# Performance work log

Hardware: AMD Instinct MI355X
Metric: run time of the kernel (lower is better)

Reference implementation:

```python
import jax, jax.numpy as jnp
import numpy as np

M = 8      # bits // 8 experts
SUB = 8    # sub-code width per expert
HID = 256  # expert output classes (2**SUB)
BITS = 64
NCLS = 100
NUM_FLIP = (BITS // 32) ** 2  # 4


def _bit_flip(x, template, key):
    # torch: rand.argsort(-1) -> shuffledTemplate = template[idx]; x[mask] *= -1
    rand = jax.random.uniform(key, x.shape)
    idx = jnp.argsort(rand, axis=-1)
    mask = template[idx]
    return jnp.where(mask, -x, x)


def _map_net(x, W1, b1, W2, b2):
    # m independent Linear(8,256)->SiLU->Linear(256,256) experts over contiguous chunks
    N = x.shape[0]
    xs = x.reshape(N, M, SUB)
    h = jax.nn.silu(jnp.einsum('nmi,mih->nmh', xs, W1) + b1)
    return jnp.einsum('nmh,mho->nmo', h, W2) + b2  # [N, M, HID]


def setup_inputs() -> dict:
    key = jax.random.key(0)
    ks = jax.random.split(key, 10)
    N = 32768
    x = jax.random.normal(ks[0], (N, BITS), jnp.float32)
    # multi-label targets, guarantee >=1 positive per row (meanWeight divides by row sum)
    y = (jax.random.uniform(ks[1], (N, NCLS)) < 0.1).astype(jnp.int32)
    lab = jax.random.randint(ks[2], (N,), 0, NCLS)
    y = y.at[jnp.arange(N), lab].set(1)
    centroids = (jax.random.uniform(ks[3], (NCLS, BITS)) > 0.5).astype(jnp.float32)
    permIdx = jax.random.permutation(ks[4], BITS)

    def make_template(k):
        t = jnp.zeros(BITS, bool).at[:NUM_FLIP].set(True)
        return jax.random.permutation(k, t)

    template_map = make_template(ks[5])
    template_raw = make_template(ks[6])
    W1 = jax.random.normal(ks[7], (M, SUB, HID), jnp.float32) / np.sqrt(SUB)
    b1 = jnp.zeros((M, HID), jnp.float32)
    W2 = jax.random.normal(ks[8], (M, HID, HID), jnp.float32) / np.sqrt(HID)
    b2 = jnp.zeros((M, HID), jnp.float32)
    return dict(x=x, y=y, centroids=centroids, permIdx=permIdx,
                template_map=template_map, template_raw=template_raw,
                W1=W1, b1=b1, W2=W2, b2=b2)


def reference(x, y, centroids, permIdx, template_map, template_raw, W1, b1, W2, b2):
    N = x.shape[0]
    multiplier = 2 ** jnp.arange(SUB)  # [8]
    kmap, kraw = jax.random.split(jax.random.key(1))

    xp = x[:, permIdx]  # permuted codes [N, BITS]
    x_det = jax.lax.stop_gradient(xp)

    # ---- mapLoss path (x detached; mapper params still trained; dropout in eval) ----
    logits_map = _map_net(_bit_flip(x_det, template_map, kmap), W1, b1, W2, b2)  # [N,M,HID]
    raw_flipped = _bit_flip(x_det, template_raw, kraw)
    binary = raw_flipped.reshape(N, M, SUB) > 0
    target = (binary * multiplier).sum(-1)  # [N, M] decimal sub-codes
    lse = jax.nn.logsumexp(logits_map, axis=-1)
    picked = jnp.take_along_axis(logits_map, target[..., None], axis=-1)[..., 0]
    mapLoss = (lse - picked).mean(0).sum()  # sum over m of per-chunk CE means
    hitRate = (logits_map.argmax(-1) == target).astype(jnp.float32).mean()

    # ---- netLoss path (mapper on non-detached x, no flip; centers detached) ----
    hashCenter = jax.lax.stop_gradient(centroids[:, permIdx])  # [C, BITS]
    centerBits = hashCenter > 0
    centerTarget = (centerBits.reshape(NCLS, M, SUB) * multiplier).sum(-1)  # [C, M]
    logits_net = _map_net(xp, W1, b1, W2, b2)  # [N, M, HID]
    lse2 = jax.nn.logsumexp(logits_net, axis=-1)  # [N, M]
    # picked2[n,m,c] = logits_net[n, m, centerTarget[c, m]]
    picked2 = logits_net[:, jnp.arange(M)[:, None], centerTarget.T]  # [N, M, C]
    ce = lse2[..., None] - picked2  # [N, M, C]
    mask = y > 0
    w = mask.astype(jnp.float32)
    w = w / w.sum(-1, keepdims=True)  # meanWeight (mask * meanWeight == meanWeight)
    netLoss = (ce * w[:, None, :]).sum() / N

    # ---- codes-to-center Hamming distance, masked mean over (n, c) with y>0 ----
    xb = (xp > 0).astype(jnp.float32)
    cb = centerBits.astype(jnp.float32)
    ham = xb.sum(-1, keepdims=True) + cb.sum(-1)[None, :] - 2.0 * (xb @ cb.T)  # [N, C]
    mf = mask.astype(jnp.float32)
    codesToCenterDistance = (ham * mf).sum() / mf.sum()

    total = netLoss + mapLoss
    return (total, netLoss, mapLoss, hitRate, codesToCenterDistance)
```

## Files before the change

### kernel.cpp

```cpp
#include <hip/hip_runtime.h>
#include <stdint.h>

#define NR 32768
#define MM 8
#define NCLS 100
#define HALFN 1048576u
#define HSS 260
#define LGS 260
#define PSS 12

#define LOG2E 1.4426950408889634f
#define LN2F  0.6931471805599453f

typedef _Float16 h8 __attribute__((ext_vector_type(8)));
typedef _Float16 h4 __attribute__((ext_vector_type(4)));
typedef float f4 __attribute__((ext_vector_type(4)));
typedef unsigned long long ull;

__host__ __device__ inline void tf2x32(uint32_t k0, uint32_t k1, uint32_t x0, uint32_t x1,
                                       uint32_t& o0, uint32_t& o1) {
  uint32_t ks0 = k0, ks1 = k1, ks2 = k0 ^ k1 ^ 0x1BD11BDAu;
  x0 += ks0; x1 += ks1;
#define TFR(r) { x0 += x1; x1 = (x1 << r) | (x1 >> (32 - r)); x1 ^= x0; }
  TFR(13) TFR(15) TFR(26) TFR(6)  x0 += ks1; x1 += ks2 + 1u;
  TFR(17) TFR(29) TFR(16) TFR(24) x0 += ks2; x1 += ks0 + 2u;
  TFR(13) TFR(15) TFR(26) TFR(6)  x0 += ks0; x1 += ks1 + 3u;
  TFR(17) TFR(29) TFR(16) TFR(24) x0 += ks1; x1 += ks2 + 4u;
  TFR(13) TFR(15) TFR(26) TFR(6)  x0 += ks2; x1 += ks0 + 5u;
#undef TFR
  o0 = x0; o1 = x1;
}

__device__ inline int load_tmpl(const void* p, int lane) {
  const unsigned* pi = (const unsigned*)p;
  unsigned w = pi[lane];
  ull okF = __ballot(w == 0u || w == 0x3F800000u);
  ull onF = __ballot(w == 0x3F800000u);
  ull okI = __ballot(w <= 1u);
  ull onI = __ballot(w == 1u);
  if (okF == ~0ull && __popcll(onF) == 4) return (w == 0x3F800000u) ? 1 : 0;
  if (okI == ~0ull && __popcll(onI) == 4) return (int)w;
  const unsigned char* pb = (const unsigned char*)p;
  return pb[lane] ? 1 : 0;
}

__device__ inline uint32_t packh2(float a, float b) {
  union { _Float16 h[2]; uint32_t u; } cv;
  cv.h[0] = (_Float16)a; cv.h[1] = (_Float16)b;
  return cv.u;
}

__device__ inline ull flip_mask(ull tmask, uint32_t key) {
  ull fm = 0;
  while (tmask) {
    int p = __ffsll((long long)tmask) - 1;
    tmask &= tmask - 1;
    uint32_t kp = (uint32_t)__builtin_amdgcn_readlane((int)key, p);
    fm |= 1ull << __popcll(__ballot(key < kp));
  }
  return fm;
}

__global__ __launch_bounds__(256) void stage1p(
    const float* __restrict__ x, const int* __restrict__ y, const int* __restrict__ perm,
    const void* tmap, const void* traw,
    uint32_t km0, uint32_t km1, uint32_t kr0, uint32_t kr1,
    const float* __restrict__ W2, const float* __restrict__ W1,
    const float* __restrict__ B1, const float* __restrict__ B2,
    const float* __restrict__ centroids,
    _Float16* __restrict__ Wp, _Float16* __restrict__ Wp1, float* __restrict__ B2s,
    ull* __restrict__ cb64,
    uint32_t* __restrict__ xp16, uint32_t* __restrict__ xm16,
    ull* __restrict__ targ, ull* __restrict__ xb,
    float* __restrict__ winv, unsigned char* __restrict__ poslist, int* __restrict__ nposA) {
  int b = blockIdx.x, tid = threadIdx.x;
  if (b >= 2048) {
    int pb = b - 2048;
    if (pb < 256) {
      int gid = pb * 256 + tid;
      int lane6 = gid & 63, frag = gid >> 6;
      int NT = frag & 15, kt = (frag >> 4) & 7, m = frag >> 7;
      int q = lane6 >> 4, lr = lane6 & 15;
      const float* src = W2 + (size_t)m * 65536 + (size_t)(kt * 32 + q * 8) * 256 + NT * 16 + lr;
      h8 v;
#pragma unroll
      for (int j = 0; j < 8; j++) v[j] = (_Float16)src[j * 256];
      *(h8*)(Wp + (size_t)gid * 8) = v;
    } else if (pb < 288) {
      int idx = (pb - 256) * 256 + tid;
      int lane = idx & 63, t = (idx >> 6) & 15, m = idx >> 10;
      int q = lane >> 4, lr = lane & 15;
      h8 v;
#pragma unroll
      for (int j = 0; j < 8; j++) {
        float val = 0.0f;
        if (q == 0) val = W1[(size_t)(m * 8 + j) * 256 + t * 16 + lr] * LOG2E;
        else if (q == 1 && j == 0) val = B1[m * 256 + t * 16 + lr] * LOG2E;
        v[j] = (_Float16)val;
      }
      *(h8*)(Wp1 + (size_t)idx * 8) = v;
    } else if (pb < 313) {
      int c = (pb - 288) * 4 + (tid >> 6);
      int lane = tid & 63;
      ull bits = __ballot(centroids[c * 64 + perm[lane]] > 0.0f);
      if (lane == 0 && c < NCLS) cb64[c] = bits;
    } else {
#pragma unroll
      for (int j = 0; j < 8; j++) B2s[tid * 8 + j] = B2[tid * 8 + j] * LOG2E;
    }
    return;
  }

  int wv = tid >> 6, lane = tid & 63;
  int tm = load_tmpl(tmap, lane);
  int tr = load_tmpl(traw, lane);
  ull tmm = __ballot(tm != 0);
  ull trm = __ballot(tr != 0);
  int pv = perm[lane];

  int nbase = b * 8 + wv * 2;
  uint32_t bmv[4], brv[4];
  {
    uint32_t iA = (uint32_t)(nbase * 64 + lane);
    uint32_t iB = iA + 64u;
    tf2x32(km0, km1, iA, iA + HALFN, bmv[0], bmv[2]);
    tf2x32(kr0, kr1, iA, iA + HALFN, brv[0], brv[2]);
    tf2x32(km0, km1, iB, iB + HALFN, bmv[1], bmv[3]);
    tf2x32(kr0, kr1, iB, iB + HALFN, brv[1], brv[3]);
  }
  const int nn[4] = {nbase, nbase + 1, nbase + 16384, nbase + 16385};
#pragma unroll
  for (int rr = 0; rr < 4; rr++) {
    int n = nn[rr];
    float xpv = x[(size_t)n * 64 + pv];
    uint32_t kmk = ((bmv[rr] >> 9) << 6) | (uint32_t)lane;
    uint32_t krk = ((brv[rr] >> 9) << 6) | (uint32_t)lane;
    ull fm = flip_mask(tmm, kmk);
    ull fr = flip_mask(trm, krk);
    float xmv = ((fm >> lane) & 1ull) ? -xpv : xpv;
    float rfv = ((fr >> lane) & 1ull) ? -xpv : xpv;
    float xp_o = __shfl_xor(xpv, 1);
    float xm_o = __shfl_xor(xmv, 1);
    if ((lane & 1) == 0) {
      xp16[n * 32 + (lane >> 1)] = packh2(xpv, xp_o);
      xm16[n * 32 + (lane >> 1)] = packh2(xmv, xm_o);
    }
    ull t64 = __ballot(rfv > 0.0f);
    ull b64v = __ballot(xpv > 0.0f);

    int c1 = y[(size_t)n * NCLS + lane] > 0;
    int c2 = (lane < NCLS - 64) ? (y[(size_t)n * NCLS + 64 + lane] > 0) : 0;
    ull p0 = __ballot(c1);
    ull p1 = __ballot(c2);
    int cnt0 = __popcll(p0);
    float cnt = (float)(cnt0 + __popcll(p1));

    unsigned char* pl = poslist + (size_t)n * 64;
    ull below = (lane == 0) ? 0ull : (~0ull >> (64 - lane));
    if (c1) pl[__popcll(p0 & below)] = (unsigned char)lane;
    if (c2) pl[cnt0 + __popcll(p1 & below)] = (unsigned char)(64 + lane);

    if (lane == 0) {
      targ[n] = t64;
      xb[n] = b64v;
      winv[n] = 1.0f / cnt;
      nposA[n] = cnt0 + __popcll(p1);
    }
  }
}

__global__ __launch_bounds__(512, 8) void mapnet8(
    const uint32_t* __restrict__ Xm16, const uint32_t* __restrict__ Xp16,
    const _Float16* __restrict__ Wp1, const _Float16* __restrict__ Wp,
    const float* __restrict__ B2s,
    const ull* __restrict__ targ, const float* __restrict__ winv,
    const unsigned char* __restrict__ poslist, const int* __restrict__ nposA,
    const ull* __restrict__ cb64, const ull* __restrict__ xb,
    float* __restrict__ accbuf) {
  __shared__ union {
    _Float16 h[64 * HSS];
    float lg[32 * LGS];
  } u;
  __shared__ float ps[64 * PSS];
  __shared__ float pm[64 * PSS];
  __shared__ float mvA[64];
  __shared__ int   tA[64];
  __shared__ float sl[3];
  const int tid = threadIdx.x, lane = tid & 63, wv = tid >> 6;
  const int q = lane >> 4, lr = lane & 15;
  const int m = blockIdx.y, pass = blockIdx.z;
  const int n0 = blockIdx.x * 64;
  if (tid < 3) sl[tid] = 0.0f;

  if (pass == 2) {
    __syncthreads();
    int flat = blockIdx.y * 512 + blockIdx.x;
    int n = flat * 8 + wv;
    ull xv = xb[n];
    float px = (float)__popcll(xv);
    int np = nposA[n];
    float hs = 0.0f;
    if (lane < np) {
      int c = poslist[(size_t)n * 64 + lane];
      ull cb = cb64[c];
      hs = px + (float)__popcll(cb) - 2.0f * (float)__popcll(xv & cb);
    }
#pragma unroll
    for (int off = 1; off < 64; off <<= 1) hs += __shfl_xor(hs, off);
    if (lane == 0) {
      atomicAdd(&sl[0], hs);
      atomicAdd(&sl[1], (float)np);
    }
    __syncthreads();
    if (tid == 0) {
      float* slot = accbuf + (flat & 127) * 8;
      atomicAdd(&slot[3], sl[0]);
      atomicAdd(&slot[4], sl[1]);
    }
    return;
  }

  const uint32_t* Xin = pass ? Xp16 : Xm16;

  const int rb = wv & 3, tbase = (wv >> 2) * 8;
  h8 af;
  {
    const _Float16* xsrc = (const _Float16*)(Xin + (size_t)(n0 + rb * 16 + lr) * 32) + m * 8;
    h8 xv = *(const h8*)xsrc;
    h8 zero = {(_Float16)0.0f, (_Float16)0.0f, (_Float16)0.0f, (_Float16)0.0f,
               (_Float16)0.0f, (_Float16)0.0f, (_Float16)0.0f, (_Float16)0.0f};
    af = (q == 0) ? xv : zero;
    if (q == 1) af[0] = (_Float16)1.0f;
  }
#pragma unroll 4
  for (int tt = 0; tt < 8; tt++) {
    int t = tbase + tt;
    h8 wfrag = *(const h8*)(Wp1 + ((size_t)(m * 16 + t) * 64 + lane) * 8);
    f4 z = __builtin_amdgcn_mfma_f32_16x16x32_f16(wfrag, af, (f4){0.f, 0.f, 0.f, 0.f}, 0, 0, 0);
    h4 pk;
#pragma unroll
    for (int reg = 0; reg < 4; reg++) {
      float z2 = z[reg];
      pk[reg] = (_Float16)(z2 * __builtin_amdgcn_rcpf(1.0f + __builtin_amdgcn_exp2f(-z2)));
    }
    *(h4*)(u.h + (size_t)(rb * 16 + lr) * HSS + t * 16 + q * 4) = pk;
  }
  __syncthreads();

  f4 acc4[4][2];
  {
    f4 bv0 = *(const f4*)(B2s + m * 256 + wv * 32 + q * 4);
    f4 bv1 = *(const f4*)(B2s + m * 256 + wv * 32 + 16 + q * 4);
#pragma unroll
    for (int rt = 0; rt < 4; rt++) { acc4[rt][0] = bv0; acc4[rt][1] = bv1; }
  }
  const size_t wbase = (size_t)m * 65536;
#pragma unroll 2
  for (int kt = 0; kt < 8; kt++) {
    h8 bh0 = *(const h8*)(Wp + wbase + (((size_t)kt * 16 + wv * 2 + 0) * 64 + lane) * 8);
    h8 bh1 = *(const h8*)(Wp + wbase + (((size_t)kt * 16 + wv * 2 + 1) * 64 + lane) * 8);
#pragma unroll
    for (int rt = 0; rt < 4; rt++) {
      const _Float16* p = u.h + (size_t)(rt * 16 + lr) * HSS + kt * 32 + q * 8;
      h4 lo = *(const h4*)p;
      h4 hi = *(const h4*)(p + 4);
      h8 ah = __builtin_shufflevector(lo, hi, 0, 1, 2, 3, 4, 5, 6, 7);
      acc4[rt][0] = __builtin_amdgcn_mfma_f32_16x16x32_f16(bh0, ah, acc4[rt][0], 0, 0, 0);
      acc4[rt][1] = __builtin_amdgcn_mfma_f32_16x16x32_f16(bh1, ah, acc4[rt][1], 0, 0, 0);
    }
  }

  float rsum[4], rmax[4];
#pragma unroll
  for (int rt = 0; rt < 4; rt++) {
    f4 l0 = acc4[rt][0], l1 = acc4[rt][1];
    float s = 0.0f;
#pragma unroll
    for (int reg = 0; reg < 4; reg++)
      s += __builtin_amdgcn_exp2f(l0[reg]) + __builtin_amdgcn_exp2f(l1[reg]);
    rsum[rt] = s;
    if (pass == 0) {
      float mv = fmaxf(l0[0], l1[0]);
#pragma unroll
      for (int reg = 1; reg < 4; reg++) mv = fmaxf(mv, fmaxf(l0[reg], l1[reg]));
      rmax[rt] = mv;
    }
  }
#pragma unroll
  for (int rt = 0; rt < 4; rt++) {
    rsum[rt] += __shfl_xor(rsum[rt], 16);
    rsum[rt] += __shfl_xor(rsum[rt], 32);
  }
  if (pass == 0) {
#pragma unroll
    for (int rt = 0; rt < 4; rt++) {
      rmax[rt] = fmaxf(rmax[rt], __shfl_xor(rmax[rt], 16));
      rmax[rt] = fmaxf(rmax[rt], __shfl_xor(rmax[rt], 32));
    }
  }
  if (lane < 16) {
#pragma unroll
    for (int rt = 0; rt < 4; rt++) {
      ps[(rt * 16 + lane) * PSS + wv] = rsum[rt];
      if (pass == 0) pm[(rt * 16 + lane) * PSS + wv] = rmax[rt];
    }
  }

  if (pass == 0) {
    __syncthreads();
    float myLse = 0.0f;
    if (tid < 64) {
      int row = tid, n = n0 + row;
      f4 s0 = *(const f4*)(ps + row * PSS);
      f4 s1 = *(const f4*)(ps + row * PSS + 4);
      f4 ss = s0 + s1;
      float s = (ss[0] + ss[1]) + (ss[2] + ss[3]);
      f4 m0 = *(const f4*)(pm + row * PSS);
      f4 m1 = *(const f4*)(pm + row * PSS + 4);
      float mv = fmaxf(fmaxf(fmaxf(m0[0], m0[1]), fmaxf(m0[2], m0[3])),
                       fmaxf(fmaxf(m1[0], m1[1]), fmaxf(m1[2], m1[3])));
      mvA[row] = mv;
      tA[row] = (int)((targ[n] >> (m * 8)) & 0xFFull);
      myLse = __builtin_amdgcn_logf(s);
    }
    __syncthreads();
    float pick = 0.0f, hit = 0.0f;
    const int cbase = wv * 32 + q * 4;
#pragma unroll
    for (int rt = 0; rt < 4; rt++) {
      int row = rt * 16 + lr;
      int d0 = tA[row] - cbase;
#pragma unroll
      for (int nt = 0; nt < 2; nt++) {
        int d = d0 - nt * 16;
        if ((unsigned)d < 4u) {
          f4 f = acc4[rt][nt];
          float v = f[0];
          v = (d == 1) ? f[1] : v;
          v = (d == 2) ? f[2] : v;
          v = (d == 3) ? f[3] : v;
          pick += v;
          hit += (v == mvA[row]) ? 1.0f : 0.0f;
        }
      }
    }
    float lossC = myLse - pick;
#pragma unroll
    for (int off = 1; off < 64; off <<= 1) {
      lossC += __shfl_xor(lossC, off);
      hit += __shfl_xor(hit, off);
    }
    if (lane == 0) {
      atomicAdd(&sl[0], lossC);
      atomicAdd(&sl[2], hit);
    }
  } else {
    float partLoss = 0.0f;
    for (int ph = 0; ph < 2; ph++) {
      __syncthreads();
#pragma unroll
      for (int rt2 = 0; rt2 < 2; rt2++) {
#pragma unroll
        for (int nt = 0; nt < 2; nt++)
#pragma unroll
          for (int reg = 0; reg < 4; reg++)
            u.lg[(rt2 * 16 + lr) * LGS + wv * 32 + nt * 16 + q * 4 + reg] =
                acc4[ph * 2 + rt2][nt][reg];
      }
      __syncthreads();
      int rl = tid >> 4;
      int grow = ph * 32 + rl;
      int n = n0 + grow;
      int cl = tid & 15;
      const float* lrow = u.lg + rl * LGS;
      int np = nposA[n];
      const unsigned char* pl = poslist + (size_t)n * 64;
      float sp = 0.0f;
      for (int j2 = cl; j2 < np; j2 += 16) {
        int c = pl[j2];
        int t = (int)((cb64[c] >> (m * 8)) & 0xFFull);
        sp += lrow[t];
      }
#pragma unroll
      for (int off = 1; off < 16; off <<= 1) sp += __shfl_xor(sp, off);
      if (cl == 0) {
        f4 s0 = *(const f4*)(ps + grow * PSS);
        f4 s1 = *(const f4*)(ps + grow * PSS + 4);
        f4 ss = s0 + s1;
        float s = (ss[0] + ss[1]) + (ss[2] + ss[3]);
        partLoss += __builtin_amdgcn_logf(s) - winv[n] * sp;
      }
    }
    partLoss += __shfl_xor(partLoss, 16);
    partLoss += __shfl_xor(partLoss, 32);
    if (lane == 0) atomicAdd(&sl[1], partLoss);
  }

  __syncthreads();
  if (tid == 0) {
    float* slot = accbuf + (blockIdx.x & 127) * 8;
    if (pass == 0) {
      atomicAdd(&slot[0], sl[0]);
      atomicAdd(&slot[2], sl[2]);
    } else {
      atomicAdd(&slot[1], sl[1]);
    }
  }
}

__global__ __launch_bounds__(128) void finalk(const float* __restrict__ accbuf, float* __restrict__ out) {
  int t = threadIdx.x;
  float v0 = accbuf[t * 8 + 0], v1 = accbuf[t * 8 + 1], v2 = accbuf[t * 8 + 2];
  float v3 = accbuf[t * 8 + 3], v4 = accbuf[t * 8 + 4];
#pragma unroll
  for (int off = 1; off < 64; off <<= 1) {
    v0 += __shfl_xor(v0, off); v1 += __shfl_xor(v1, off); v2 += __shfl_xor(v2, off);
    v3 += __shfl_xor(v3, off); v4 += __shfl_xor(v4, off);
  }
  __shared__ float s[2][5];
  if ((t & 63) == 0) {
    s[t >> 6][0] = v0; s[t >> 6][1] = v1; s[t >> 6][2] = v2; s[t >> 6][3] = v3; s[t >> 6][4] = v4;
  }
  __syncthreads();
  if (t == 0) {
    float a0 = s[0][0] + s[1][0], a1 = s[0][1] + s[1][1], a2 = s[0][2] + s[1][2];
    float a3 = s[0][3] + s[1][3], a4 = s[0][4] + s[1][4];
    float netLoss = a1 * LN2F / (float)NR;
    float mapLoss = a0 * LN2F / (float)NR;
    out[0] = netLoss + mapLoss;
    out[1] = netLoss;
    out[2] = mapLoss;
    out[3] = a2 / (float)(NR * MM);
    out[4] = a3 / a4;
  }
}

extern "C" void kernel_launch(void* const* d_in, const int* in_sizes, int n_in,
                              void* d_out, int out_size, void* d_ws, size_t ws_size,
                              hipStream_t stream) {
  const float* x = (const float*)d_in[0];
  const int* y = (const int*)d_in[1];
  const float* centroids = (const float*)d_in[2];
  const int* perm = (const int*)d_in[3];
  const void* tmap = d_in[4];
  const void* traw = d_in[5];
  const float* W1 = (const float*)d_in[6];
  const float* B1 = (const float*)d_in[7];
  const float* W2 = (const float*)d_in[8];
  const float* B2 = (const float*)d_in[9];
  float* out = (float*)d_out;

  char* w = (char*)d_ws;
  float* accbuf = (float*)w;
  uint32_t* xp16 = (uint32_t*)(w + 4096);
  uint32_t* xm16 = xp16 + (size_t)NR * 32;
  ull* targ = (ull*)(xm16 + (size_t)NR * 32);
  ull* cb64 = targ + NR;
  ull* xb = cb64 + 128;
  float* winv = (float*)(xb + NR);
  int* nposA = (int*)(winv + NR);
  unsigned char* poslist = (unsigned char*)(nposA + NR);
  _Float16* Wp = (_Float16*)(poslist + (size_t)NR * 64);
  _Float16* Wp1 = Wp + (1 << 19);
  float* B2s = (float*)(Wp1 + (1 << 16));

  hipMemsetAsync(accbuf, 0, 4096, stream);

  uint32_t a0, b0, a1, b1;
  tf2x32(0u, 1u, 0u, 2u, a0, b0);
  tf2x32(0u, 1u, 1u, 3u, a1, b1);

  stage1p<<<2048 + 314, 256, 0, stream>>>(x, y, perm, tmap, traw, a0, a1, b0, b1,
                                          W2, W1, B1, B2, centroids, Wp, Wp1, B2s, cb64,
                                          xp16, xm16, targ, xb, winv, poslist, nposA);
  dim3 g(NR / 64, MM, 3);
  mapnet8<<<g, 512, 0, stream>>>(xm16, xp16, Wp1, Wp, B2s, targ, winv, poslist, nposA,
                                 cb64, xb, accbuf);
  finalk<<<1, 128, 0, stream>>>(accbuf, out);
}
```

Baseline: 214.4 us.

## Fold Hamming-distance pass into mapnet blocks and batch stage1 global loads

Removes the separate third grid slice that computed the codes-to-center Hamming sum. That work now runs inside the pass-0, expert-0 mapnet blocks, with each wave handling 8 rows before the MFMA work. It also hoists the x and y loads in stage1p into a first loop so all four rows' loads are issued before use. This cuts grid size and lets memory loads overlap, at the cost of extra work and load imbalance in 512 of the blocks.

Result: no change. 212.0 us (-1.1%).

```diff
diff --git a/kernel.cpp b/kernel.cpp
--- a/kernel.cpp
+++ b/kernel.cpp
@@ -129,10 +129,19 @@
     tf2x32(kr0, kr1, iB, iB + HALFN, brv[1], brv[3]);
   }
   const int nn[4] = {nbase, nbase + 1, nbase + 16384, nbase + 16385};
+  float xr[4];
+  int yv1[4], yv2[4];
 #pragma unroll
   for (int rr = 0; rr < 4; rr++) {
     int n = nn[rr];
-    float xpv = x[(size_t)n * 64 + pv];
+    xr[rr] = x[(size_t)n * 64 + pv];
+    yv1[rr] = y[(size_t)n * NCLS + lane];
+    yv2[rr] = (lane < NCLS - 64) ? y[(size_t)n * NCLS + 64 + lane] : 0;
+  }
+#pragma unroll
+  for (int rr = 0; rr < 4; rr++) {
+    int n = nn[rr];
+    float xpv = xr[rr];
     uint32_t kmk = ((bmv[rr] >> 9) << 6) | (uint32_t)lane;
     uint32_t krk = ((brv[rr] >> 9) << 6) | (uint32_t)lane;
     ull fm = flip_mask(tmm, kmk);
@@ -148,8 +157,8 @@
     ull t64 = __ballot(rfv > 0.0f);
     ull b64v = __ballot(xpv > 0.0f);
 
-    int c1 = y[(size_t)n * NCLS + lane] > 0;
-    int c2 = (lane < NCLS - 64) ? (y[(size_t)n * NCLS + 64 + lane] > 0) : 0;
+    int c1 = yv1[rr] > 0;
+    int c2 = yv2[rr] > 0;
     ull p0 = __ballot(c1);
     ull p1 = __ballot(c2);
     int cnt0 = __popcll(p0);
@@ -185,42 +194,39 @@
   __shared__ float pm[64 * PSS];
   __shared__ float mvA[64];
   __shared__ int   tA[64];
-  __shared__ float sl[3];
+  __shared__ float sl[6];
   const int tid = threadIdx.x, lane = tid & 63, wv = tid >> 6;
   const int q = lane >> 4, lr = lane & 15;
   const int m = blockIdx.y, pass = blockIdx.z;
   const int n0 = blockIdx.x * 64;
-  if (tid < 3) sl[tid] = 0.0f;
-
-  if (pass == 2) {
-    __syncthreads();
-    int flat = blockIdx.y * 512 + blockIdx.x;
-    int n = flat * 8 + wv;
-    ull xv = xb[n];
-    float px = (float)__popcll(xv);
-    int np = nposA[n];
-    float hs = 0.0f;
-    if (lane < np) {
-      int c = poslist[(size_t)n * 64 + lane];
-      ull cb = cb64[c];
-      hs = px + (float)__popcll(cb) - 2.0f * (float)__popcll(xv & cb);
-    }
-#pragma unroll
-    for (int off = 1; off < 64; off <<= 1) hs += __shfl_xor(hs, off);
-    if (lane == 0) {
-      atomicAdd(&sl[0], hs);
-      atomicAdd(&sl[1], (float)np);
-    }
-    __syncthreads();
-    if (tid == 0) {
-      float* slot = accbuf + (flat & 127) * 8;
-      atomicAdd(&slot[3], sl[0]);
-      atomicAdd(&slot[4], sl[1]);
-    }
-    return;
-  }
+  if (tid < 6) sl[tid] = 0.0f;
 
   const uint32_t* Xin = pass ? Xp16 : Xm16;
+  const bool doHam = (pass == 0) && (m == 0);
+
+  float hamS = 0.0f, npS = 0.0f;
+  if (doHam) {
+    ull xv[8];
+    int np[8];
+    unsigned char pc[8];
+    const int nh = n0 + wv * 8;
+#pragma unroll
+    for (int r = 0; r < 8; r++) {
+      xv[r] = xb[nh + r];
+      np[r] = nposA[nh + r];
+      pc[r] = poslist[(size_t)(nh + r) * 64 + lane];
+    }
+#pragma unroll
+    for (int r = 0; r < 8; r++) {
+      if (lane < np[r]) {
+        ull cb = cb64[pc[r]];
+        hamS += (float)__popcll(xv[r]) + (float)__popcll(cb) - 2.0f * (float)__popcll(xv[r] & cb);
+      }
+      npS += (float)np[r];
+    }
+#pragma unroll
+    for (int off = 1; off < 64; off <<= 1) hamS += __shfl_xor(hamS, off);
+  }
 
   const int rb = wv & 3, tbase = (wv >> 2) * 8;
   h8 af;
@@ -353,6 +359,10 @@
     if (lane == 0) {
       atomicAdd(&sl[0], lossC);
       atomicAdd(&sl[2], hit);
+      if (doHam) {
+        atomicAdd(&sl[3], hamS);
+        atomicAdd(&sl[4], npS);
+      }
     }
   } else {
     float partLoss = 0.0f;
@@ -402,6 +412,10 @@
     if (pass == 0) {
       atomicAdd(&slot[0], sl[0]);
       atomicAdd(&slot[2], sl[2]);
+      if (doHam) {
+        atomicAdd(&slot[3], sl[3]);
+        atomicAdd(&slot[4], sl[4]);
+      }
     } else {
       atomicAdd(&slot[1], sl[1]);
     }
@@ -473,7 +487,7 @@
   stage1p<<<2048 + 314, 256, 0, stream>>>(x, y, perm, tmap, traw, a0, a1, b0, b1,
                                           W2, W1, B1, B2, centroids, Wp, Wp1, B2s, cb64,
                                           xp16, xm16, targ, xb, winv, poslist, nposA);
-  dim3 g(NR / 64, MM, 3);
+  dim3 g(NR / 64, MM, 2);
   mapnet8<<<g, 512, 0, stream>>>(xm16, xp16, Wp1, Wp, B2s, targ, winv, poslist, nposA,
                                  cb64, xb, accbuf);
   finalk<<<1, 128, 0, stream>>>(accbuf, out);
```
